# Performance work log

Hardware: AMD Instinct MI355X
Metric: run time of the kernel (lower is better)

## Reference

```python
import jax, jax.numpy as jnp
import numpy as np

N_CLASSES = 16
GAMMA = 2.0
MULT_UNLABELED = 3.0
EPS = 1e-6
B, C, D, H, W, K = 2, 16, 64, 128, 128, 4


def setup_inputs() -> dict:
    key = jax.random.key(0)
    k1, k2, k3 = jax.random.split(key, 3)
    # probs are softmax outputs over the class axis (axis=1)
    probs = jax.nn.softmax(jax.random.normal(k1, (B, C, D, H, W), dtype=jnp.float32), axis=1)
    target = jax.random.randint(k2, (B, D, H, W), 0, N_CLASSES, dtype=jnp.int32)
    annotated_fg_categories = jax.random.randint(k3, (B, K), 0, N_CLASSES, dtype=jnp.int32)
    return {"probs": probs, "target": target, "annotated_fg_categories": annotated_fg_categories}


def reference(probs, target, annotated_fg_categories):
    # ---- regularization: -mean_spatial( sum_c p * log(clamp(p)) ) per sample ----
    logp = jnp.log(jnp.clip(probs, EPS, 1.0 - EPS))
    ent = jnp.mean(jnp.sum(probs * logp, axis=1), axis=(1, 2, 3))  # [B]
    all_bg = jnp.all(target == 0, axis=(1, 2, 3))                  # sample fully unlabeled?
    mult = jnp.where(all_bg, MULT_UNLABELED, 1.0)
    batch = target.shape[0]
    reg = -jnp.sum(mult * ent) / batch

    # ---- balanced focal CE ----
    # Every voxel belongs to exactly one unique label of its patch, so the
    # per-unique-label concat + mean in the torch loop equals a per-voxel mean.
    classes = jnp.arange(N_CLASSES)
    ann = annotated_fg_categories
    annotated = jnp.any((ann[:, :, None] == classes[None, None, :]) & (ann[:, :, None] > 0), axis=1)  # [B,C]
    unannot = (~annotated).astype(probs.dtype)  # includes class 0 (never annotated as fg)
    # background voxels: p = sum of probs over unannotated categories
    s0 = jnp.einsum('bcdhw,bc->bdhw', probs, unannot)
    # foreground voxels: p = probs at the target class
    p_fg = jnp.take_along_axis(probs, target[:, None].astype(jnp.int32), axis=1)[:, 0]
    p = jnp.where(target > 0, p_fg, s0)  # [B,D,H,W]
    # focal term uses unclamped p; log is clamped (matches torch code)
    ce_vox = -jnp.power(1.0 - p, GAMMA) * jnp.log(jnp.clip(p, EPS, 1.0 - EPS))
    ce = jnp.mean(ce_vox)  # mean over voxels == mean of per-sample means (equal voxel counts)
    return (ce, reg)
```

## Files before the change

### kernel.cpp

```cpp
#include <hip/hip_runtime.h>
#include <math.h>

#define SPATIAL (64 * 128 * 128)
#define NCLS 16
#define NB 2
#define NBLK 2048
#define TPB 256


typedef float  f32x4 __attribute__((ext_vector_type(4)));
typedef int    i32x4 __attribute__((ext_vector_type(4)));

__device__ __forceinline__ f32x4 ntload4(const float* p) {
    return __builtin_nontemporal_load(reinterpret_cast<const f32x4*>(p));
}
__device__ __forceinline__ i32x4 ntload4i(const int* p) {
    return __builtin_nontemporal_load(reinterpret_cast<const i32x4*>(p));
}

__global__ __launch_bounds__(TPB) void bce_main(
    const float* __restrict__ probs,
    const int*   __restrict__ target,
    const int*   __restrict__ ann,
    float*       __restrict__ partials)
{
    const int j = blockIdx.x * TPB + threadIdx.x;
    const int v = j * 4;
    const int b = v >> 20;
    const int s = v & (SPATIAL - 1);
    const int rot = blockIdx.x & 3;

    const i32x4 t4 = ntload4i(target + v);
    const int t[4] = {t4.x, t4.y, t4.z, t4.w};

    unsigned a = 0;
#pragma unroll
    for (int k = 0; k < 4; ++k) {
        const int c = ann[b * 4 + k];
        if (c > 0) a |= (1u << c);
    }
    const unsigned m = ~a & 0xFFFFu;

    const float* pb = probs + (size_t)b * NCLS * SPATIAL + s;

    float ent[4] = {0.f, 0.f, 0.f, 0.f};
    float s0[4]  = {0.f, 0.f, 0.f, 0.f};
    float pt[4]  = {0.f, 0.f, 0.f, 0.f};

    f32x4 buf[2][4];
    {
        const int ck0 = rot;
#pragma unroll
        for (int c = 0; c < 4; ++c)
            buf[0][c] = ntload4(pb + (size_t)(ck0 * 4 + c) * SPATIAL);
    }

#pragma unroll
    for (int ch = 0; ch < 4; ++ch) {
        const int cur = ch & 1, nxt = cur ^ 1;
        if (ch < 3) {
            const int ckn = (ch + 1 + rot) & 3;
#pragma unroll
            for (int c = 0; c < 4; ++c)
                buf[nxt][c] = ntload4(pb + (size_t)(ckn * 4 + c) * SPATIAL);
        }
        const int ck = (ch + rot) & 3;
#pragma unroll
        for (int c = 0; c < 4; ++c) {
            const int cls = ck * 4 + c;
            const float p[4] = {buf[cur][c].x, buf[cur][c].y, buf[cur][c].z, buf[cur][c].w};
            const bool un = (m >> cls) & 1u;
#pragma unroll
            for (int q = 0; q < 4; ++q) {
                const float pc = fminf(fmaxf(p[q], 1e-6f), 0.999999f);
                ent[q] = fmaf(p[q], __log2f(pc), ent[q]);
                if (un) s0[q] += p[q];
                if (cls == t[q]) pt[q] = p[q];
            }
        }
    }

    float ce_sum = 0.f, ent_b = 0.f, cnt_b = 0.f;
#pragma unroll
    for (int q = 0; q < 4; ++q) {
        const float p  = (t[q] > 0) ? pt[q] : s0[q];
        const float pc = fminf(fmaxf(p, 1e-6f), 0.999999f);
        const float om = 1.f - p;
        ce_sum += om * om * __log2f(pc);
        ent_b  += ent[q];
        cnt_b  += (t[q] != 0) ? 1.f : 0.f;
    }

    float vals[5];
    vals[0] = ce_sum;
    vals[1] = (b == 0) ? ent_b : 0.f;
    vals[2] = (b == 1) ? ent_b : 0.f;
    vals[3] = (b == 0) ? cnt_b : 0.f;
    vals[4] = (b == 1) ? cnt_b : 0.f;

    __shared__ float red[5][TPB / 64];
    const int lane = threadIdx.x & 63;
    const int wave = threadIdx.x >> 6;
#pragma unroll
    for (int qq = 0; qq < 5; ++qq) {
        float x = vals[qq];
#pragma unroll
        for (int off = 32; off > 0; off >>= 1)
            x += __shfl_down(x, off, 64);
        if (lane == 0) red[qq][wave] = x;
    }
    __syncthreads();
    if (threadIdx.x == 0) {
#pragma unroll
        for (int qq = 0; qq < 5; ++qq) {
            float x = 0.f;
#pragma unroll
            for (int w = 0; w < TPB / 64; ++w) x += red[qq][w];
            partials[qq * NBLK + blockIdx.x] = x;
        }
    }
}

__global__ __launch_bounds__(64) void bce_final(
    const float* __restrict__ partials, float* __restrict__ out)
{
    const int lane = threadIdx.x;
    float acc[5] = {0.f, 0.f, 0.f, 0.f, 0.f};
#pragma unroll
    for (int qq = 0; qq < 5; ++qq) {
        const float4* src = reinterpret_cast<const float4*>(partials + qq * NBLK);
#pragma unroll
        for (int i = 0; i < 8; ++i) {
            const float4 x = src[i * 64 + lane];
            acc[qq] += (x.x + x.y) + (x.z + x.w);
        }
    }
#pragma unroll
    for (int qq = 0; qq < 5; ++qq) {
#pragma unroll
        for (int off = 32; off > 0; off >>= 1)
            acc[qq] += __shfl_down(acc[qq], off, 64);
    }
    if (lane == 0) {
        const float ce = acc[0], e0 = acc[1], e1 = acc[2], c0 = acc[3], c1 = acc[4];
        const float LN2  = 0.69314718055994530942f;
        const float invS = 1.f / (float)SPATIAL;
        const float ent0 = e0 * LN2 * invS;
        const float ent1 = e1 * LN2 * invS;
        const float m0   = (c0 == 0.f) ? 3.f : 1.f;
        const float m1   = (c1 == 0.f) ? 3.f : 1.f;
        out[0] = -(ce * LN2) / (float)(NB * SPATIAL);
        out[1] = -(m0 * ent0 + m1 * ent1) * 0.5f;
    }
}

extern "C" void kernel_launch(void* const* d_in, const int* in_sizes, int n_in,
                              void* d_out, int out_size, void* d_ws, size_t ws_size,
                              hipStream_t stream) {
    const float* probs  = (const float*)d_in[0];
    const int*   target = (const int*)d_in[1];
    const int*   ann    = (const int*)d_in[2];
    float*       out    = (float*)d_out;
    float*       partials = (float*)d_ws;

    bce_main<<<NBLK, TPB, 0, stream>>>(probs, target, ann, partials);
    bce_final<<<1, 64, 0, stream>>>(partials, out);
}
```

Measured before the change: 33.79 us.

## Split class planes across waves and combine per-voxel sums via LDS

Each block now covers a 512-voxel window, and each wave handles 4 of the 16 class planes for that window. Each thread works on two float4 chunks per plane instead of one thread walking all 16 planes. Per-voxel entropy and selected-probability partials are combined across waves through shared memory before the focal term is computed. This doubles the block count and shortens each thread's serial dependency chain and load stream, at the cost of LDS traffic, an extra barrier and a second read of the target.

```diff
diff --git a/kernel.cpp b/kernel.cpp
--- a/kernel.cpp
+++ b/kernel.cpp
@@ -4,7 +4,8 @@
 #define SPATIAL (64 * 128 * 128)
 #define NCLS 16
 #define NB 2
-#define NBLK 2048
+#define WIN 512
+#define NBLK 4096
 #define TPB 256
 
 
@@ -18,77 +19,87 @@
     return __builtin_nontemporal_load(reinterpret_cast<const i32x4*>(p));
 }
 
-__global__ __launch_bounds__(TPB) void bce_main(
+__global__ __launch_bounds__(TPB) void bce_planar(
     const float* __restrict__ probs,
     const int*   __restrict__ target,
     const int*   __restrict__ ann,
     float*       __restrict__ partials)
 {
-    const int j = blockIdx.x * TPB + threadIdx.x;
-    const int v = j * 4;
-    const int b = v >> 20;
-    const int s = v & (SPATIAL - 1);
-    const int rot = blockIdx.x & 3;
+    const int wbg  = blockIdx.x * WIN;
+    const int b    = wbg >> 20;
+    const int s    = wbg & (SPATIAL - 1);
+    const int wave = threadIdx.x >> 6;
+    const int lane = threadIdx.x & 63;
 
-    const i32x4 t4 = ntload4i(target + v);
-    const int t[4] = {t4.x, t4.y, t4.z, t4.w};
-
-    unsigned a = 0;
+    unsigned am = 0;
 #pragma unroll
     for (int k = 0; k < 4; ++k) {
         const int c = ann[b * 4 + k];
-        if (c > 0) a |= (1u << c);
+        if (c > 0) am |= (1u << c);
     }
-    const unsigned m = ~a & 0xFFFFu;
+    const unsigned m = ~am & 0xFFFFu;
 
-    const float* pb = probs + (size_t)b * NCLS * SPATIAL + s;
+    const int la = 4 * lane;
+    const int lb = 256 + 4 * lane;
 
-    float ent[4] = {0.f, 0.f, 0.f, 0.f};
-    float s0[4]  = {0.f, 0.f, 0.f, 0.f};
-    float pt[4]  = {0.f, 0.f, 0.f, 0.f};
+    const i32x4 tA = ntload4i(target + wbg + la);
+    const i32x4 tB = ntload4i(target + wbg + lb);
+    const int ta[4] = {tA.x, tA.y, tA.z, tA.w};
+    const int tb[4] = {tB.x, tB.y, tB.z, tB.w};
 
-    f32x4 buf[2][4];
-    {
-        const int ck0 = rot;
-#pragma unroll
-        for (int c = 0; c < 4; ++c)
-            buf[0][c] = ntload4(pb + (size_t)(ck0 * 4 + c) * SPATIAL);
-    }
+    const float* pw = probs + (size_t)b * NCLS * SPATIAL + (size_t)(wave * 4) * SPATIAL + s;
+
+    float entA[4] = {0.f, 0.f, 0.f, 0.f}, pfA[4] = {0.f, 0.f, 0.f, 0.f};
+    float entB[4] = {0.f, 0.f, 0.f, 0.f}, pfB[4] = {0.f, 0.f, 0.f, 0.f};
+
+    f32x4 bufA[2], bufB[2];
+    bufA[0] = ntload4(pw + la);
+    bufB[0] = ntload4(pw + lb);
 
 #pragma unroll
-    for (int ch = 0; ch < 4; ++ch) {
-        const int cur = ch & 1, nxt = cur ^ 1;
-        if (ch < 3) {
-            const int ckn = (ch + 1 + rot) & 3;
+    for (int k = 0; k < 4; ++k) {
+        const int cur = k & 1, nxt = cur ^ 1;
+        if (k < 3) {
+            bufA[nxt] = ntload4(pw + (size_t)(k + 1) * SPATIAL + la);
+            bufB[nxt] = ntload4(pw + (size_t)(k + 1) * SPATIAL + lb);
+        }
+        const int cls = wave * 4 + k;
+        const bool un = (m >> cls) & 1u;
+        const float pA[4] = {bufA[cur].x, bufA[cur].y, bufA[cur].z, bufA[cur].w};
+        const float pB[4] = {bufB[cur].x, bufB[cur].y, bufB[cur].z, bufB[cur].w};
 #pragma unroll
-            for (int c = 0; c < 4; ++c)
-                buf[nxt][c] = ntload4(pb + (size_t)(ckn * 4 + c) * SPATIAL);
-        }
-        const int ck = (ch + rot) & 3;
-#pragma unroll
-        for (int c = 0; c < 4; ++c) {
-            const int cls = ck * 4 + c;
-            const float p[4] = {buf[cur][c].x, buf[cur][c].y, buf[cur][c].z, buf[cur][c].w};
-            const bool un = (m >> cls) & 1u;
-#pragma unroll
-            for (int q = 0; q < 4; ++q) {
-                const float pc = fminf(fmaxf(p[q], 1e-6f), 0.999999f);
-                ent[q] = fmaf(p[q], __log2f(pc), ent[q]);
-                if (un) s0[q] += p[q];
-                if (cls == t[q]) pt[q] = p[q];
-            }
+        for (int q = 0; q < 4; ++q) {
+            const float pcA = fminf(fmaxf(pA[q], 1e-6f), 0.999999f);
+            entA[q] = fmaf(pA[q], __log2f(pcA), entA[q]);
+            const float pcB = fminf(fmaxf(pB[q], 1e-6f), 0.999999f);
+            entB[q] = fmaf(pB[q], __log2f(pcB), entB[q]);
+            pfA[q] += (ta[q] > 0) ? ((cls == ta[q]) ? pA[q] : 0.f)
+                                  : (un ? pA[q] : 0.f);
+            pfB[q] += (tb[q] > 0) ? ((cls == tb[q]) ? pB[q] : 0.f)
+                                  : (un ? pB[q] : 0.f);
         }
     }
 
+    __shared__ float lent[4][WIN];
+    __shared__ float lpf [4][WIN];
+    *reinterpret_cast<f32x4*>(&lent[wave][la]) = f32x4{entA[0], entA[1], entA[2], entA[3]};
+    *reinterpret_cast<f32x4*>(&lent[wave][lb]) = f32x4{entB[0], entB[1], entB[2], entB[3]};
+    *reinterpret_cast<f32x4*>(&lpf [wave][la]) = f32x4{pfA[0], pfA[1], pfA[2], pfA[3]};
+    *reinterpret_cast<f32x4*>(&lpf [wave][lb]) = f32x4{pfB[0], pfB[1], pfB[2], pfB[3]};
+    __syncthreads();
+
     float ce_sum = 0.f, ent_b = 0.f, cnt_b = 0.f;
 #pragma unroll
-    for (int q = 0; q < 4; ++q) {
-        const float p  = (t[q] > 0) ? pt[q] : s0[q];
-        const float pc = fminf(fmaxf(p, 1e-6f), 0.999999f);
-        const float om = 1.f - p;
+    for (int h = 0; h < 2; ++h) {
+        const int v = threadIdx.x + h * 256;
+        const float ENT = ((lent[0][v] + lent[1][v]) + (lent[2][v] + lent[3][v]));
+        const float p   = ((lpf[0][v] + lpf[1][v]) + (lpf[2][v] + lpf[3][v]));
+        const int   t   = target[wbg + v];
+        const float pc  = fminf(fmaxf(p, 1e-6f), 0.999999f);
+        const float om  = 1.f - p;
         ce_sum += om * om * __log2f(pc);
-        ent_b  += ent[q];
-        cnt_b  += (t[q] != 0) ? 1.f : 0.f;
+        ent_b  += ENT;
+        cnt_b  += (t != 0) ? 1.f : 0.f;
     }
 
     float vals[5];
@@ -99,8 +110,6 @@
     vals[4] = (b == 1) ? cnt_b : 0.f;
 
     __shared__ float red[5][TPB / 64];
-    const int lane = threadIdx.x & 63;
-    const int wave = threadIdx.x >> 6;
 #pragma unroll
     for (int qq = 0; qq < 5; ++qq) {
         float x = vals[qq];
@@ -130,7 +139,7 @@
     for (int qq = 0; qq < 5; ++qq) {
         const float4* src = reinterpret_cast<const float4*>(partials + qq * NBLK);
 #pragma unroll
-        for (int i = 0; i < 8; ++i) {
+        for (int i = 0; i < 16; ++i) {
             const float4 x = src[i * 64 + lane];
             acc[qq] += (x.x + x.y) + (x.z + x.w);
         }
@@ -163,6 +172,6 @@
     float*       out    = (float*)d_out;
     float*       partials = (float*)d_ws;
 
-    bce_main<<<NBLK, TPB, 0, stream>>>(probs, target, ann, partials);
+    bce_planar<<<NBLK, TPB, 0, stream>>>(probs, target, ann, partials);
     bce_final<<<1, 64, 0, stream>>>(partials, out);
 }
```

Result: slower. 36.80 us (+8.9%).
